# Optimization experiments

Measured on AMD Instinct MI355X. Metric: run time of the kernel, lower is better.

## Reference

```python
import jax, jax.numpy as jnp
import numpy as np

NUM_HEADS = 12
D = 768
HD = D // NUM_HEADS  # 64

def setup_inputs() -> dict:
    key = jax.random.key(0)
    ks = jax.random.split(key, 9)
    s = 0.02
    return {
        "x": jax.random.normal(ks[0], (4, 2048, D), dtype=jnp.float32),
        "QW_w": jax.random.normal(ks[1], (D, D), dtype=jnp.float32) * s,
        "QW_b": jax.random.normal(ks[2], (D,), dtype=jnp.float32) * s,
        "KW_w": jax.random.normal(ks[3], (D, D), dtype=jnp.float32) * s,
        "KW_b": jax.random.normal(ks[4], (D,), dtype=jnp.float32) * s,
        "VW_w": jax.random.normal(ks[5], (D, D), dtype=jnp.float32) * s,
        "VW_b": jax.random.normal(ks[6], (D,), dtype=jnp.float32) * s,
        "OW_w": jax.random.normal(ks[7], (D, D), dtype=jnp.float32) * s,
        "OW_b": jax.random.normal(ks[8], (D,), dtype=jnp.float32) * s,
    }

def reference(x, QW_w, QW_b, KW_w, KW_b, VW_w, VW_b, OW_w, OW_b):
    b, s, _ = x.shape
    # torch nn.Linear: y = x @ W.T + b
    def proj(w, bias):
        y = jnp.einsum('bsd,ed->bse', x, w) + bias
        return y.reshape(b, s, NUM_HEADS, HD).transpose(0, 2, 1, 3)  # [b,h,s,hd]
    q = proj(QW_w, QW_b)
    k = proj(KW_w, KW_b)
    v = proj(VW_w, VW_b)
    scores = jnp.einsum('bhqd,bhkd->bhqk', q, k) / jnp.sqrt(jnp.float32(HD))
    attn = jax.nn.softmax(scores, axis=-1)
    out = jnp.einsum('bhqk,bhkd->bhqd', attn, v)
    out = out.transpose(0, 2, 1, 3).reshape(b, s, NUM_HEADS * HD)
    return jnp.einsum('bsd,ed->bse', out, OW_w) + OW_b
```

## Files before the change

kernel.cpp:

```cpp
#include <hip/hip_runtime.h>
#include <hip/hip_bf16.h>

#define NH  12
#define HD  64
#define DIM 768
#define SEQ 2048
#define NB  4
#define MM  (NB*SEQ)
#define NKB (SEQ/64)

typedef short    v8s  __attribute__((ext_vector_type(8)));
typedef float    v4f  __attribute__((ext_vector_type(4)));
typedef float    v16f __attribute__((ext_vector_type(16)));
typedef unsigned v4u  __attribute__((ext_vector_type(4)));

#if __has_builtin(__builtin_amdgcn_exp2f)
#define EXP2(x) __builtin_amdgcn_exp2f(x)
#else
#define EXP2(x) __builtin_exp2f(x)
#endif

static __device__ __forceinline__ unsigned short f2b(float f) {
    unsigned int u = __float_as_uint(f);
    return (unsigned short)((u + 0x7FFFu + ((u >> 16) & 1u)) >> 16);
}
static __device__ __forceinline__ unsigned cvtpk(float lo, float hi) {
    unsigned r;
    asm("v_cvt_pk_bf16_f32 %0, %1, %2" : "=v"(r) : "v"(lo), "v"(hi));
    return r;
}
static __device__ __forceinline__ void g2l16(const unsigned short* g, unsigned short* l) {
    __builtin_amdgcn_global_load_lds(
        (const __attribute__((address_space(1))) void*)g,
        (__attribute__((address_space(3))) void*)l, 16, 0, 0);
}

__global__ void cast_f32_bf16(const float* __restrict__ in,
                              unsigned short* __restrict__ out, int n4) {
    int i = blockIdx.x * blockDim.x + threadIdx.x;
    if (i < n4) {
        float4 v = reinterpret_cast<const float4*>(in)[i];
        ushort4 o;
        o.x = f2b(v.x); o.y = f2b(v.y); o.z = f2b(v.z); o.w = f2b(v.w);
        reinterpret_cast<ushort4*>(out)[i] = o;
    }
}

__global__ void cast4_f32_bf16(const float* __restrict__ i0, const float* __restrict__ i1,
                               const float* __restrict__ i2, const float* __restrict__ i3,
                               unsigned short* __restrict__ o0, unsigned short* __restrict__ o1,
                               unsigned short* __restrict__ o2, unsigned short* __restrict__ o3,
                               int n4) {
    int i = blockIdx.x * blockDim.x + threadIdx.x;
    if (i >= n4) return;
    const float* in; unsigned short* out;
    switch (blockIdx.y) {
        case 0: in = i0; out = o0; break;
        case 1: in = i1; out = o1; break;
        case 2: in = i2; out = o2; break;
        default: in = i3; out = o3; break;
    }
    float4 v = reinterpret_cast<const float4*>(in)[i];
    ushort4 o;
    o.x = f2b(v.x); o.y = f2b(v.y); o.z = f2b(v.z); o.w = f2b(v.w);
    reinterpret_cast<ushort4*>(out)[i] = o;
}

__global__ __launch_bounds__(256, 3) void gemm_qkv(
    const unsigned short* __restrict__ A,
    const unsigned short* __restrict__ Wq,
    const unsigned short* __restrict__ Wk,
    const unsigned short* __restrict__ Wv,
    const float* __restrict__ bq,
    const float* __restrict__ bk,
    const float* __restrict__ bvp,
    unsigned short* __restrict__ Qb,
    unsigned short* __restrict__ Kfo,
    unsigned short* __restrict__ Vf)
{
    __shared__ __align__(16) unsigned short As[128 * 64];
    __shared__ __align__(16) unsigned short Bs[3][64 * 64];

    const int tid  = threadIdx.x;
    const int w    = tid >> 6, lane = tid & 63;
    const int quad = lane >> 4, l16 = lane & 15;
    const int wm   = w & 1,  wn = w >> 1;
    const int lane8 = lane >> 3, sc = lane & 7;
    const int m0   = blockIdx.x * 128;
    const int h    = blockIdx.y;
    const int n0   = h * 64;

    v4f acc[3][4][2];
    #pragma unroll
    for (int s = 0; s < 3; ++s)
        #pragma unroll
        for (int i = 0; i < 4; ++i)
            #pragma unroll
            for (int j = 0; j < 2; ++j)
                acc[s][i][j] = v4f{0.f, 0.f, 0.f, 0.f};

    for (int kb = 0; kb < DIM; kb += 64) {
        __syncthreads();
        #pragma unroll
        for (int t = 0; t < 4; ++t) {
            int r8 = w * 32 + t * 8;
            int r  = r8 + lane8;
            int gch = sc ^ (r & 7);
            g2l16(&A[(size_t)(m0 + r) * DIM + kb + gch * 8], &As[r8 * 64]);
        }
        #pragma unroll
        for (int u = 0; u < 6; ++u) {
            int G = w * 6 + u;
            int set = G >> 3, rg = G & 7;
            int row = rg * 8 + lane8;
            int gch = sc ^ (row & 7);
            const unsigned short* Wp = (set == 0) ? Wq : (set == 1) ? Wk : Wv;
            g2l16(&Wp[(size_t)(n0 + row) * DIM + kb + gch * 8], &Bs[set][rg * 8 * 64]);
        }
        __syncthreads();
        #pragma unroll
        for (int kk = 0; kk < 64; kk += 32) {
            int chb = kk >> 3;
            v8s a[4];
            #pragma unroll
            for (int i = 0; i < 4; ++i) {
                int m = wm * 64 + i * 16 + l16;
                a[i] = *reinterpret_cast<const v8s*>(
                    &As[m * 64 + (((chb + quad) ^ (m & 7)) << 3)]);
            }
            #pragma unroll
            for (int s = 0; s < 3; ++s) {
                v8s b[2];
                #pragma unroll
                for (int j = 0; j < 2; ++j) {
                    int n = wn * 32 + j * 16 + l16;
                    b[j] = *reinterpret_cast<const v8s*>(
                        &Bs[s][n * 64 + (((chb + quad) ^ (n & 7)) << 3)]);
                }
                #pragma unroll
                for (int i = 0; i < 4; ++i)
                    #pragma unroll
                    for (int j = 0; j < 2; ++j)
                        acc[s][i][j] = __builtin_amdgcn_mfma_f32_16x16x32_bf16(
                            a[i], b[j], acc[s][i][j], 0, 0, 0);
            }
        }
    }

    #pragma unroll
    for (int i = 0; i < 4; ++i) {
        #pragma unroll
        for (int j = 0; j < 2; ++j) {
            int hd = wn * 32 + j * 16 + l16;
            float bias_v = bq[n0 + hd];
            #pragma unroll
            for (int r = 0; r < 4; ++r) {
                int gm = m0 + wm * 64 + i * 16 + quad * 4 + r;
                int bb = gm >> 11, sq = gm & (SEQ - 1);
                Qb[((size_t)(bb * NH + h) * SEQ + sq) * HD + hd] =
                    f2b((acc[0][i][j][r] + bias_v) * 0.1803368801f);
            }
        }
    }
    #pragma unroll
    for (int i = 0; i < 4; ++i) {
        int kh = i >> 1;
        #pragma unroll
        for (int j = 0; j < 2; ++j) {
            int hd = wn * 32 + j * 16 + l16;
            int c  = hd >> 4;
            int half_a = (l16 >> 3) & 1;
            int jj = l16 & 7;
            float bias_v = bk[n0 + hd];
            int gm0 = m0 + wm * 64 + i * 16 + quad * 4;
            int bb = gm0 >> 11, sk = gm0 & (SEQ - 1);
            int t = sk >> 6;
            int l31k = (i & 1) * 16 + quad * 4;
            size_t frag = ((size_t)(bb * NH + h) * NKB + t) * 8 + kh * 4 + c;
            unsigned short* dst = &Kfo[frag * 512 + (half_a * 32 + l31k) * 8 + jj];
            #pragma unroll
            for (int r = 0; r < 4; ++r)
                dst[r * 8] = f2b(acc[1][i][j][r] + bias_v);
        }
    }
    #pragma unroll
    for (int i = 0; i < 4; ++i) {
        #pragma unroll
        for (int j = 0; j < 2; ++j) {
            int hd = wn * 32 + j * 16 + l16;
            int hb = hd >> 5, l31v = hd & 31;
            float bias_v = bvp[n0 + hd];
            int gm0 = m0 + wm * 64 + i * 16 + quad * 4;
            int bb = gm0 >> 11, sk = gm0 & (SEQ - 1);
            int kbi = sk >> 6;
            int halfv = quad >> 1, j0 = (quad & 1) * 4;
            ushort4 pkv;
            pkv.x = f2b(acc[2][i][j][0] + bias_v);
            pkv.y = f2b(acc[2][i][j][1] + bias_v);
            pkv.z = f2b(acc[2][i][j][2] + bias_v);
            pkv.w = f2b(acc[2][i][j][3] + bias_v);
            size_t frag = ((size_t)(bb * NH + h) * NKB + kbi) * 8 + hb * 4 + i;
            *reinterpret_cast<ushort4*>(
                &Vf[frag * 512 + (halfv * 32 + l31v) * 8 + j0]) = pkv;
        }
    }
}

__global__ __launch_bounds__(256, 3) void gemm_o(
    const unsigned short* __restrict__ A,
    const unsigned short* __restrict__ W,
    const float* __restrict__ bias,
    float* __restrict__ out)
{
    __shared__ __align__(16) unsigned short As[128 * 64];
    __shared__ __align__(16) unsigned short Bs[64 * 64];

    const int tid  = threadIdx.x;
    const int w    = tid >> 6, lane = tid & 63;
    const int quad = lane >> 4, l16 = lane & 15;
    const int wm   = w & 1,  wn = w >> 1;
    const int lane8 = lane >> 3, sc = lane & 7;
    const int m0  = blockIdx.x * 128;
    const int n0l = blockIdx.y * 64;

    v4f acc[4][2];
    #pragma unroll
    for (int i = 0; i < 4; ++i)
        #pragma unroll
        for (int j = 0; j < 2; ++j)
            acc[i][j] = v4f{0.f, 0.f, 0.f, 0.f};

    for (int kb = 0; kb < DIM; kb += 64) {
        __syncthreads();
        #pragma unroll
        for (int t = 0; t < 4; ++t) {
            int r8 = w * 32 + t * 8;
            int r  = r8 + lane8;
            int gch = sc ^ (r & 7);
            g2l16(&A[(size_t)(m0 + r) * DIM + kb + gch * 8], &As[r8 * 64]);
        }
        #pragma unroll
        for (int t = 0; t < 2; ++t) {
            int r8 = (w * 2 + t) * 8;
            int r  = r8 + lane8;
            int gch = sc ^ (r & 7);
            g2l16(&W[(size_t)(n0l + r) * DIM + kb + gch * 8], &Bs[r8 * 64]);
        }
        __syncthreads();
        #pragma unroll
        for (int kk = 0; kk < 64; kk += 32) {
            v8s a[4], b[2];
            int chb = kk >> 3;
            #pragma unroll
            for (int i = 0; i < 4; ++i) {
                int m = wm * 64 + i * 16 + l16;
                a[i] = *reinterpret_cast<const v8s*>(
                    &As[m * 64 + (((chb + quad) ^ (m & 7)) << 3)]);
            }
            #pragma unroll
            for (int j = 0; j < 2; ++j) {
                int n = wn * 32 + j * 16 + l16;
                b[j] = *reinterpret_cast<const v8s*>(
                    &Bs[n * 64 + (((chb + quad) ^ (n & 7)) << 3)]);
            }
            #pragma unroll
            for (int i = 0; i < 4; ++i)
                #pragma unroll
                for (int j = 0; j < 2; ++j)
                    acc[i][j] = __builtin_amdgcn_mfma_f32_16x16x32_bf16(a[i], b[j], acc[i][j], 0, 0, 0);
        }
    }

    #pragma unroll
    for (int i = 0; i < 4; ++i) {
        #pragma unroll
        for (int j = 0; j < 2; ++j) {
            int gn = n0l + wn * 32 + j * 16 + l16;
            float bias_v = bias[gn];
            #pragma unroll
            for (int r = 0; r < 4; ++r) {
                int gm = m0 + wm * 64 + i * 16 + quad * 4 + r;
                out[(size_t)gm * DIM + gn] = acc[i][j][r] + bias_v;
            }
        }
    }
}

__global__ __launch_bounds__(256, 3) void attn(
    const unsigned short* __restrict__ Q,
    const unsigned short* __restrict__ Kf,
    const unsigned short* __restrict__ Vf,
    unsigned short* __restrict__ ctx)
{
    const int tid  = threadIdx.x;
    const int w    = tid >> 6, lane = tid & 63;
    const int l31  = lane & 31, half = lane >> 5;

    const int lblk = blockIdx.y * 16 + blockIdx.x;
    const int vblk = (lblk & 7) * 96 + (lblk >> 3);
    const int bh   = vblk >> 4;
    const int b    = bh / NH, h = bh % NH;
    const int q0   = (vblk & 15) * 128 + w * 32;

    const unsigned short* Qp = Q  + ((size_t)bh * SEQ + q0) * HD;
    const unsigned short* Kh = Kf + (size_t)bh * (NKB * 8 * 512) + lane * 8;
    const unsigned short* Vh = Vf + (size_t)bh * (NKB * 8 * 512) + lane * 8;

    v8s bq[4];
    #pragma unroll
    for (int c = 0; c < 4; ++c)
        bq[c] = *reinterpret_cast<const v8s*>(&Qp[l31 * HD + c * 16 + half * 8]);

    v8s ka[2][4], va[2][4];
    #pragma unroll
    for (int g = 0; g < 8; ++g)
        reinterpret_cast<v8s*>(ka)[g] = *reinterpret_cast<const v8s*>(&Kh[(size_t)g * 512]);
    #pragma unroll
    for (int g = 0; g < 8; ++g)
        reinterpret_cast<v8s*>(va)[g] = *reinterpret_cast<const v8s*>(&Vh[(size_t)g * 512]);

    v16f o0a, o0b, o1a, o1b, Z;
    #pragma unroll
    for (int i = 0; i < 16; ++i) {
        o0a[i] = 0.f; o0b[i] = 0.f; o1a[i] = 0.f; o1b[i] = 0.f; Z[i] = 0.f;
    }
    float li = 0.f;

    for (int it = 0; it < NKB; ++it) {
        v16f s0 = __builtin_amdgcn_mfma_f32_32x32x16_bf16(ka[0][0], bq[0], Z, 0, 0, 0);
        v16f s1 = __builtin_amdgcn_mfma_f32_32x32x16_bf16(ka[1][0], bq[0], Z, 0, 0, 0);
        #pragma unroll
        for (int c = 1; c < 4; ++c) {
            s0 = __builtin_amdgcn_mfma_f32_32x32x16_bf16(ka[0][c], bq[c], s0, 0, 0, 0);
            s1 = __builtin_amdgcn_mfma_f32_32x32x16_bf16(ka[1][c], bq[c], s1, 0, 0, 0);
        }

        {
            int nt = (it + 1 < NKB) ? it + 1 : it;
            #pragma unroll
            for (int g = 0; g < 8; ++g)
                reinterpret_cast<v8s*>(ka)[g] =
                    *reinterpret_cast<const v8s*>(&Kh[((size_t)nt * 8 + g) * 512]);
        }

        unsigned pk[8][2];
        #pragma unroll
        for (int g = 0; g < 4; ++g) {
            float e0 = EXP2(s0[4*g+0]), e1 = EXP2(s0[4*g+1]);
            float e2 = EXP2(s0[4*g+2]), e3 = EXP2(s0[4*g+3]);
            li += (e0 + e1) + (e2 + e3);
            pk[g][0] = cvtpk(e0, e1);
            pk[g][1] = cvtpk(e2, e3);
            float f0 = EXP2(s1[4*g+0]), f1 = EXP2(s1[4*g+1]);
            float f2 = EXP2(s1[4*g+2]), f3 = EXP2(s1[4*g+3]);
            li += (f0 + f1) + (f2 + f3);
            pk[4+g][0] = cvtpk(f0, f1);
            pk[4+g][1] = cvtpk(f2, f3);
        }

        #pragma unroll
        for (int cp = 0; cp < 4; ++cp) {
            unsigned a0 = pk[2*cp][0],   a1 = pk[2*cp][1];
            unsigned b0 = pk[2*cp+1][0], b1 = pk[2*cp+1][1];
            asm("v_permlane32_swap_b32 %0, %1" : "+v"(a0), "+v"(b0));
            asm("v_permlane32_swap_b32 %0, %1" : "+v"(a1), "+v"(b1));
            v4u fw;
            fw.x = a0; fw.y = a1; fw.z = b0; fw.w = b1;
            v8s pf = __builtin_bit_cast(v8s, fw);
            if (cp < 2) {
                o0a = __builtin_amdgcn_mfma_f32_32x32x16_bf16(va[0][cp], pf, o0a, 0, 0, 0);
                o1a = __builtin_amdgcn_mfma_f32_32x32x16_bf16(va[1][cp], pf, o1a, 0, 0, 0);
            } else {
                o0b = __builtin_amdgcn_mfma_f32_32x32x16_bf16(va[0][cp], pf, o0b, 0, 0, 0);
                o1b = __builtin_amdgcn_mfma_f32_32x32x16_bf16(va[1][cp], pf, o1b, 0, 0, 0);
            }
        }

        {
            int nt = (it + 1 < NKB) ? it + 1 : it;
            #pragma unroll
            for (int g = 0; g < 8; ++g)
                reinterpret_cast<v8s*>(va)[g] =
                    *reinterpret_cast<const v8s*>(&Vh[((size_t)nt * 8 + g) * 512]);
        }
    }

    float inv = 1.0f / (li + __shfl_xor(li, 32));

    const int q = q0 + l31;
    size_t base = ((size_t)(b * SEQ + q)) * DIM + h * HD;
    #pragma unroll
    for (int g = 0; g < 4; ++g) {
        int hd0 = 8 * g + 4 * half;
        uint2 u0, u1;
        u0.x = cvtpk((o0a[4*g+0] + o0b[4*g+0]) * inv, (o0a[4*g+1] + o0b[4*g+1]) * inv);
        u0.y = cvtpk((o0a[4*g+2] + o0b[4*g+2]) * inv, (o0a[4*g+3] + o0b[4*g+3]) * inv);
        u1.x = cvtpk((o1a[4*g+0] + o1b[4*g+0]) * inv, (o1a[4*g+1] + o1b[4*g+1]) * inv);
        u1.y = cvtpk((o1a[4*g+2] + o1b[4*g+2]) * inv, (o1a[4*g+3] + o1b[4*g+3]) * inv);
        *reinterpret_cast<uint2*>(&ctx[base + hd0])      = u0;
        *reinterpret_cast<uint2*>(&ctx[base + 32 + hd0]) = u1;
    }
}

extern "C" void kernel_launch(void* const* d_in, const int* in_sizes, int n_in,
                              void* d_out, int out_size, void* d_ws, size_t ws_size,
                              hipStream_t stream) {
    const float* x  = (const float*)d_in[0];
    const float* qw = (const float*)d_in[1]; const float* qb = (const float*)d_in[2];
    const float* kw = (const float*)d_in[3]; const float* kb = (const float*)d_in[4];
    const float* vw = (const float*)d_in[5]; const float* vb = (const float*)d_in[6];
    const float* ow = (const float*)d_in[7]; const float* ob = (const float*)d_in[8];
    float* out = (float*)d_out;

    char* ws = (char*)d_ws;
    size_t off = 0;
    auto alloc = [&](size_t bytes) -> unsigned short* {
        unsigned short* p = (unsigned short*)(ws + off);
        off += (bytes + 255) & ~(size_t)255;
        return p;
    };
    const size_t XB = (size_t)MM * DIM * 2;
    const size_t WB = (size_t)DIM * DIM * 2;
    const size_t QB = (size_t)NB * NH * SEQ * HD * 2;

    unsigned short* xb  = alloc(XB);
    unsigned short* wqb = alloc(WB);
    unsigned short* wkb = alloc(WB);
    unsigned short* wvb = alloc(WB);
    unsigned short* wob = alloc(WB);
    unsigned short* Qb  = alloc(QB);
    unsigned short* Kfb = alloc(QB);
    unsigned short* Vfb = alloc(QB);
    unsigned short* ctx = alloc(XB);

    const int n4x = MM * DIM / 4;
    const int n4w = DIM * DIM / 4;
    cast_f32_bf16<<<(n4x + 255) / 256, 256, 0, stream>>>(x, xb, n4x);
    cast4_f32_bf16<<<dim3((n4w + 255) / 256, 4), 256, 0, stream>>>(
        qw, kw, vw, ow, wqb, wkb, wvb, wob, n4w);

    gemm_qkv<<<dim3(MM / 128, NH), 256, 0, stream>>>(
        xb, wqb, wkb, wvb, qb, kb, vb, Qb, Kfb, Vfb);

    attn<<<dim3(SEQ / 128, NB * NH), 256, 0, stream>>>(Qb, Kfb, Vfb, ctx);

    gemm_o<<<dim3(MM / 128, DIM / 64), 256, 0, stream>>>(ctx, wob, ob, out);
}
```

Baseline: 207.5 us.

## Stage K/V tiles into double-buffered LDS shared across waves in attention

Previously each of the four waves in an attention block loaded the full K and V tiles from global memory into registers for every key block. Now each wave loads a quarter of each tile into a double-buffered shared-memory buffer using the g2l16 helper, and all waves then read their MFMA operands from LDS. The intent is to cut global/L2 traffic for K/V by sharing it across the block and to overlap the next tile's load with the current compute. In exchange it adds a __syncthreads per iteration, LDS reads on the critical path, and 32KB of LDS per block, which could limit occupancy.

```diff
diff --git a/kernel.cpp b/kernel.cpp
--- a/kernel.cpp
+++ b/kernel.cpp
@@ -292,6 +292,9 @@
     const unsigned short* __restrict__ Vf,
     unsigned short* __restrict__ ctx)
 {
+    __shared__ __align__(16) unsigned short Ks[2][8 * 512];
+    __shared__ __align__(16) unsigned short Vs[2][8 * 512];
+
     const int tid  = threadIdx.x;
     const int w    = tid >> 6, lane = tid & 63;
     const int l31  = lane & 31, half = lane >> 5;
@@ -303,21 +306,27 @@
     const int q0   = (vblk & 15) * 128 + w * 32;
 
     const unsigned short* Qp = Q  + ((size_t)bh * SEQ + q0) * HD;
-    const unsigned short* Kh = Kf + (size_t)bh * (NKB * 8 * 512) + lane * 8;
-    const unsigned short* Vh = Vf + (size_t)bh * (NKB * 8 * 512) + lane * 8;
+    const unsigned short* Kh = Kf + (size_t)bh * (NKB * 8 * 512);
+    const unsigned short* Vh = Vf + (size_t)bh * (NKB * 8 * 512);
 
     v8s bq[4];
     #pragma unroll
     for (int c = 0; c < 4; ++c)
         bq[c] = *reinterpret_cast<const v8s*>(&Qp[l31 * HD + c * 16 + half * 8]);
 
-    v8s ka[2][4], va[2][4];
-    #pragma unroll
-    for (int g = 0; g < 8; ++g)
-        reinterpret_cast<v8s*>(ka)[g] = *reinterpret_cast<const v8s*>(&Kh[(size_t)g * 512]);
-    #pragma unroll
-    for (int g = 0; g < 8; ++g)
-        reinterpret_cast<v8s*>(va)[g] = *reinterpret_cast<const v8s*>(&Vh[(size_t)g * 512]);
+    #define STAGE(it_, buf_)                                                   \
+        do {                                                                   \
+            _Pragma("unroll")                                                  \
+            for (int t = 0; t < 2; ++t) {                                      \
+                int g = w * 2 + t;                                             \
+                g2l16(&Kh[((size_t)(it_) * 8 + g) * 512 + lane * 8],           \
+                      &Ks[buf_][g * 512]);                                     \
+                g2l16(&Vh[((size_t)(it_) * 8 + g) * 512 + lane * 8],           \
+                      &Vs[buf_][g * 512]);                                     \
+            }                                                                  \
+        } while (0)
+
+    STAGE(0, 0);
 
     v16f o0a, o0b, o1a, o1b, Z;
     #pragma unroll
@@ -326,21 +335,27 @@
     }
     float li = 0.f;
 
+    int cur = 0;
     for (int it = 0; it < NKB; ++it) {
-        v16f s0 = __builtin_amdgcn_mfma_f32_32x32x16_bf16(ka[0][0], bq[0], Z, 0, 0, 0);
-        v16f s1 = __builtin_amdgcn_mfma_f32_32x32x16_bf16(ka[1][0], bq[0], Z, 0, 0, 0);
-        #pragma unroll
-        for (int c = 1; c < 4; ++c) {
-            s0 = __builtin_amdgcn_mfma_f32_32x32x16_bf16(ka[0][c], bq[c], s0, 0, 0, 0);
-            s1 = __builtin_amdgcn_mfma_f32_32x32x16_bf16(ka[1][c], bq[c], s1, 0, 0, 0);
-        }
-
+        __syncthreads();
+        if (it + 1 < NKB) STAGE(it + 1, cur ^ 1);
+
+        const unsigned short* Kb_ = Ks[cur];
+        const unsigned short* Vb_ = Vs[cur];
+
+        v16f s0, s1;
         {
-            int nt = (it + 1 < NKB) ? it + 1 : it;
-            #pragma unroll
-            for (int g = 0; g < 8; ++g)
-                reinterpret_cast<v8s*>(ka)[g] =
-                    *reinterpret_cast<const v8s*>(&Kh[((size_t)nt * 8 + g) * 512]);
+            v8s k0 = *reinterpret_cast<const v8s*>(&Kb_[lane * 8]);
+            v8s k1 = *reinterpret_cast<const v8s*>(&Kb_[4 * 512 + lane * 8]);
+            s0 = __builtin_amdgcn_mfma_f32_32x32x16_bf16(k0, bq[0], Z, 0, 0, 0);
+            s1 = __builtin_amdgcn_mfma_f32_32x32x16_bf16(k1, bq[0], Z, 0, 0, 0);
+            #pragma unroll
+            for (int c = 1; c < 4; ++c) {
+                v8s kc0 = *reinterpret_cast<const v8s*>(&Kb_[(size_t)c * 512 + lane * 8]);
+                v8s kc1 = *reinterpret_cast<const v8s*>(&Kb_[(size_t)(4 + c) * 512 + lane * 8]);
+                s0 = __builtin_amdgcn_mfma_f32_32x32x16_bf16(kc0, bq[c], s0, 0, 0, 0);
+                s1 = __builtin_amdgcn_mfma_f32_32x32x16_bf16(kc1, bq[c], s1, 0, 0, 0);
+            }
         }
 
         unsigned pk[8][2];
@@ -367,23 +382,20 @@
             v4u fw;
             fw.x = a0; fw.y = a1; fw.z = b0; fw.w = b1;
             v8s pf = __builtin_bit_cast(v8s, fw);
+            v8s v0 = *reinterpret_cast<const v8s*>(&Vb_[(size_t)cp * 512 + lane * 8]);
+            v8s v1 = *reinterpret_cast<const v8s*>(&Vb_[(size_t)(4 + cp) * 512 + lane * 8]);
             if (cp < 2) {
-                o0a = __builtin_amdgcn_mfma_f32_32x32x16_bf16(va[0][cp], pf, o0a, 0, 0, 0);
-                o1a = __builtin_amdgcn_mfma_f32_32x32x16_bf16(va[1][cp], pf, o1a, 0, 0, 0);
+                o0a = __builtin_amdgcn_mfma_f32_32x32x16_bf16(v0, pf, o0a, 0, 0, 0);
+                o1a = __builtin_amdgcn_mfma_f32_32x32x16_bf16(v1, pf, o1a, 0, 0, 0);
             } else {
-                o0b = __builtin_amdgcn_mfma_f32_32x32x16_bf16(va[0][cp], pf, o0b, 0, 0, 0);
-                o1b = __builtin_amdgcn_mfma_f32_32x32x16_bf16(va[1][cp], pf, o1b, 0, 0, 0);
-            }
-        }
-
-        {
-            int nt = (it + 1 < NKB) ? it + 1 : it;
-            #pragma unroll
-            for (int g = 0; g < 8; ++g)
-                reinterpret_cast<v8s*>(va)[g] =
-                    *reinterpret_cast<const v8s*>(&Vh[((size_t)nt * 8 + g) * 512]);
-        }
-    }
+                o0b = __builtin_amdgcn_mfma_f32_32x32x16_bf16(v0, pf, o0b, 0, 0, 0);
+                o1b = __builtin_amdgcn_mfma_f32_32x32x16_bf16(v1, pf, o1b, 0, 0, 0);
+            }
+        }
+
+        cur ^= 1;
+    }
+    #undef STAGE
 
     float inv = 1.0f / (li + __shfl_xor(li, 32));
 
```

Measured after the change: 205.3 us. About the same (-1.1%).
